# Kernel tuning notes

Measured on AMD Instinct MI355X. Metric: run time of the kernel, lower is better.

## Reference

```python
import jax, jax.numpy as jnp
import numpy as np

B, N, E, H = 4, 2048, 512, 8
D = E // H  # head dim = 64


def setup_inputs() -> dict:
    key = jax.random.key(0)
    ks = jax.random.split(key, 5)
    s = 1.0 / np.sqrt(E)
    return {
        "x": jax.random.normal(ks[0], (B, N, E), dtype=jnp.float32),
        "Wk": jax.random.normal(ks[1], (E, E), dtype=jnp.float32) * s,
        "bk": jax.random.normal(ks[2], (E,), dtype=jnp.float32) * s,
        "Wv": jax.random.normal(ks[3], (E, E), dtype=jnp.float32) * s,
        "bv": jax.random.normal(ks[4], (E,), dtype=jnp.float32) * s,
    }


def reference(x, Wk, bk, Wv, bv):
    b, n, e = x.shape
    # Linear projections (torch Linear: y = x @ W.T + b), split into heads.
    keys = (x @ Wk.T + bk).reshape(b, n, H, D).transpose(0, 2, 1, 3)    # b h n d
    values = (x @ Wv.T + bv).reshape(b, n, H, D).transpose(0, 2, 1, 3)  # b h n d
    # Q = K self-attention: scores [b, h, n, n]
    dotprod = jnp.einsum('bhnd,bhmd->bhnm', keys, keys)
    # softmax over last axis, then unusual POST-softmax scaling by sqrt(emb)
    att = jax.nn.softmax(dotprod, axis=-1) / jnp.sqrt(jnp.asarray(e, x.dtype))
    # dropout p=0 -> identity
    out = jnp.einsum('bhnm,bhmd->bhnd', att, values)
    return out.transpose(0, 2, 1, 3).reshape(b, n, e)
```

## Files before the change

kernel.cpp:

```cpp
#include <hip/hip_runtime.h>

typedef __bf16 bf16_t;
typedef bf16_t bf16x8 __attribute__((ext_vector_type(8)));
typedef float f32x4 __attribute__((ext_vector_type(4)));

#define NSEQ 2048
#define EMB 512
#define HEADS 8
#define HD 64
#define BATCH 4
#define LOG2E 1.4426950408889634f

#define MFMA16(a, b, c) __builtin_amdgcn_mfma_f32_16x16x32_bf16(a, b, c, 0, 0, 0)


__global__ __launch_bounds__(256, 2) void proj_kernel(
    const float* __restrict__ x,
    const float* __restrict__ Wk, const float* __restrict__ bk,
    const float* __restrict__ Wv, const float* __restrict__ bv,
    bf16_t* __restrict__ Kf, bf16_t* __restrict__ Vf)
{
  __shared__ union {
    struct {
      __align__(16) bf16_t A[2][128][40];
      __align__(16) bf16_t B[2][128][40];
    } s;
    __align__(16) bf16_t T[128][136];
  } u;

  const int t    = threadIdx.x;
  const int w    = t >> 6;
  const int lane = t & 63;
  const int quad = lane >> 4;
  const int l15  = lane & 15;
  const int wr   = w >> 1, wc = w & 1;
  const int m0   = blockIdx.x * 128;
  const int n0   = blockIdx.y * 128;
  const int zz   = (blockIdx.y >= 4);
  const float* __restrict__ W = zz ? Wv : Wk;
  const int nW = n0 - zz * 512;

  const int sr = t >> 3;
  const int sj = t & 7;
  const int sb = sj >> 2, sc = (sj & 3) * 8;

  float4 pa[4][2], pb[4][2];
  auto prefetch = [&](int k0) {
#pragma unroll
    for (int i = 0; i < 4; ++i) {
      const float* xa = x + (size_t)(m0 + sr + i * 32) * EMB + k0 + sj * 8;
      const float* wa = W + (size_t)(nW + sr + i * 32) * EMB + k0 + sj * 8;
      pa[i][0] = *(const float4*)xa; pa[i][1] = *(const float4*)(xa + 4);
      pb[i][0] = *(const float4*)wa; pb[i][1] = *(const float4*)(wa + 4);
    }
  };
  auto pack8 = [](float4 a, float4 b) -> bf16x8 {
    bf16x8 v;
    v[0] = (bf16_t)a.x; v[1] = (bf16_t)a.y; v[2] = (bf16_t)a.z; v[3] = (bf16_t)a.w;
    v[4] = (bf16_t)b.x; v[5] = (bf16_t)b.y; v[6] = (bf16_t)b.z; v[7] = (bf16_t)b.w;
    return v;
  };

  f32x4 acc[4][4] = {};
  prefetch(0);

  for (int it = 0; it < 8; ++it) {
    __syncthreads();
#pragma unroll
    for (int i = 0; i < 4; ++i) {
      *(bf16x8*)(&u.s.A[sb][sr + i * 32][sc]) = pack8(pa[i][0], pa[i][1]);
      *(bf16x8*)(&u.s.B[sb][sr + i * 32][sc]) = pack8(pb[i][0], pb[i][1]);
    }
    __syncthreads();
    if (it < 7) prefetch((it + 1) * 64);

    bf16x8 af[4][2], bf[4][2];
#pragma unroll
    for (int mt = 0; mt < 4; ++mt)
#pragma unroll
      for (int kk = 0; kk < 2; ++kk)
        af[mt][kk] = *(const bf16x8*)(&u.s.A[kk][wr * 64 + mt * 16 + l15][quad * 8]);
#pragma unroll
    for (int nt = 0; nt < 4; ++nt)
#pragma unroll
      for (int kk = 0; kk < 2; ++kk)
        bf[nt][kk] = *(const bf16x8*)(&u.s.B[kk][wc * 64 + nt * 16 + l15][quad * 8]);
#pragma unroll
    for (int kk = 0; kk < 2; ++kk)
#pragma unroll
      for (int mt = 0; mt < 4; ++mt)
#pragma unroll
        for (int nt = 0; nt < 4; ++nt)
          acc[mt][nt] = MFMA16(af[mt][kk], bf[nt][kk], acc[mt][nt]);
  }

  __syncthreads();

#pragma unroll
  for (int mt = 0; mt < 4; ++mt) {
#pragma unroll
    for (int nt = 0; nt < 4; ++nt) {
      const int F = wc * 64 + nt * 16 + l15;
      const int c = n0 + F;
      const float bb = zz ? bv[c - 512] : bk[c];
#pragma unroll
      for (int reg = 0; reg < 4; ++reg) {
        const int R = wr * 64 + mt * 16 + quad * 4 + reg;
        const float v = acc[mt][nt][reg] + bb;
        if (!zz) u.T[R][F] = (bf16_t)v;
        else     u.T[F][R] = (bf16_t)v;
      }
    }
  }
  __syncthreads();

  if (!zz) {
#pragma unroll
    for (int i = 0; i < 8; ++i) {
      const int fi  = i * 4 + w;
      const int hL  = fi >> 4, kk = (fi >> 3) & 1, ktl = fi & 7;
      const bf16x8 v = *(const bf16x8*)(&u.T[ktl * 16 + l15][hL * 64 + kk * 32 + quad * 8]);
      const int gr = m0 + ktl * 16 + l15;
      const int b = gr >> 11, n = gr & (NSEQ - 1);
      const int bh = b * HEADS + (n0 >> 6) + hL;
      bf16_t* dst = Kf + (((size_t)(bh * 128 + (n >> 4)) * 2 + kk)) * 512 + lane * 8;
      *(bf16x8*)dst = v;
    }
  } else {
#pragma unroll
    for (int i = 0; i < 8; ++i) {
      const int fi   = i * 4 + w;
      const int hL   = fi >> 4, dt = (fi >> 2) & 3, k32l = fi & 3;
      const bf16x8 v = *(const bf16x8*)(&u.T[hL * 64 + dt * 16 + l15][k32l * 32 + quad * 8]);
      const int gr = m0 + k32l * 32;
      const int b = gr >> 11, n = gr & (NSEQ - 1);
      const int bh = b * HEADS + ((n0 - 512) >> 6) + hL;
      bf16_t* dst = Vf + (((size_t)(bh * 64 + (n >> 5)) * 4 + dt)) * 512 + lane * 8;
      *(bf16x8*)dst = v;
    }
  }
}

__global__ __launch_bounds__(256, 2) void flash_kernel(
    const bf16_t* __restrict__ Kf, const bf16_t* __restrict__ Vf,
    float* __restrict__ out)
{
  __shared__ union {
    __align__(16) bf16_t Pl[4][64][40];
    struct {
      __align__(16) float Cb[2][4096];
      __align__(16) float Lb[2][64][16];
    } c;
  } u;

  const int t    = threadIdx.x;
  const int w    = t >> 6;
  const int lane = t & 63;
  const int quad = lane >> 4;
  const int l15  = lane & 15;
  const int rh   = w & 1;
  const int kh   = w >> 1;

  const int bh = blockIdx.x;
  const int b  = bh >> 3, h = bh & 7;
  const int rowbase = blockIdx.y * 128 + rh * 64;
  const int qtile   = rowbase >> 4;

  const bf16_t* __restrict__ Kb = Kf + (size_t)bh * 128 * 2 * 512;
  const bf16_t* __restrict__ Vb = Vf + (size_t)bh * 64 * 4 * 512;

  bf16x8 qf[4][2];
#pragma unroll
  for (int nt = 0; nt < 4; ++nt)
#pragma unroll
    for (int kk = 0; kk < 2; ++kk)
      qf[nt][kk] = *(const bf16x8*)(Kb + ((size_t)(qtile + nt) * 2 + kk) * 512 + lane * 8);

  float mlog[4];
#pragma unroll
  for (int nt = 0; nt < 4; ++nt) {
    float ss = 0.f;
#pragma unroll
    for (int kk = 0; kk < 2; ++kk)
#pragma unroll
      for (int j = 0; j < 8; ++j) {
        const float qv = (float)qf[nt][kk][j];
        ss = fmaf(qv, qv, ss);
      }
    ss += __shfl_xor(ss, 16, 64);
    ss += __shfl_xor(ss, 32, 64);
    mlog[nt] = ss * LOG2E;
  }

  bf16x8 ones;
#pragma unroll
  for (int j = 0; j < 8; ++j) ones[j] = (bf16_t)1.0f;

  f32x4 acco[4][4] = {};
  f32x4 accll[4]   = {};

  auto load_k = [&](int kt, bf16x8 (&dst)[2][2]) {
    const int kb = kt * 4 + kh * 2;
#pragma unroll
    for (int jt = 0; jt < 2; ++jt)
#pragma unroll
      for (int kk = 0; kk < 2; ++kk)
        dst[jt][kk] =
            *(const bf16x8*)(Kb + ((size_t)(kb + jt) * 2 + kk) * 512 + lane * 8);
  };

  auto body = [&](int kt, bf16x8 (&kcur)[2][2], bf16x8 (&knxt)[2][2]) {
    bf16x8 vf[4];
    const int v32 = kt * 2 + kh;
#pragma unroll
    for (int dt = 0; dt < 4; ++dt)
      vf[dt] = *(const bf16x8*)(Vb + ((size_t)v32 * 4 + dt) * 512 + lane * 8);

    f32x4 st[2][4] = {};
#pragma unroll
    for (int kk = 0; kk < 2; ++kk)
#pragma unroll
      for (int jt = 0; jt < 2; ++jt)
#pragma unroll
        for (int nt = 0; nt < 4; ++nt)
          st[jt][nt] = MFMA16(kcur[jt][kk], qf[nt][kk], st[jt][nt]);

    load_k(kt + 1 < NSEQ / 64 ? kt + 1 : kt, knxt);

#pragma unroll
    for (int jt = 0; jt < 2; ++jt)
#pragma unroll
      for (int nt = 0; nt < 4; ++nt) {
        union { bf16_t hx[4]; uint2 u2; } pw;
#pragma unroll
        for (int reg = 0; reg < 4; ++reg) {
          const float p =
              __builtin_amdgcn_exp2f(fmaf(st[jt][nt][reg], LOG2E, -mlog[nt]));
          pw.hx[reg] = (bf16_t)p;
        }
        *(uint2*)(&u.Pl[w][nt * 16 + l15][jt * 16 + quad * 4]) = pw.u2;
      }

    bf16x8 pf[4];
#pragma unroll
    for (int rt = 0; rt < 4; ++rt)
      pf[rt] = *(const bf16x8*)(&u.Pl[w][rt * 16 + l15][quad * 8]);
#pragma unroll
    for (int rt = 0; rt < 4; ++rt) {
      accll[rt] = MFMA16(pf[rt], ones, accll[rt]);
#pragma unroll
      for (int dt = 0; dt < 4; ++dt)
        acco[rt][dt] = MFMA16(pf[rt], vf[dt], acco[rt][dt]);
    }
  };

  bf16x8 kA[2][2], kB[2][2];
  load_k(0, kA);
  for (int kt = 0; kt < NSEQ / 64; kt += 2) {
    body(kt,     kA, kB);
    body(kt + 1, kB, kA);
  }

  __syncthreads();
  if (kh == 1) {
#pragma unroll
    for (int rt = 0; rt < 4; ++rt) {
#pragma unroll
      for (int dt = 0; dt < 4; ++dt)
        *(f32x4*)(&u.c.Cb[rh][((rt * 4 + dt) * 64 + lane) * 4]) = acco[rt][dt];
      *(f32x4*)(&u.c.Lb[rh][lane][rt * 4]) = accll[rt];
    }
  }
  __syncthreads();
  if (kh == 0) {
#pragma unroll
    for (int rt = 0; rt < 4; ++rt) {
#pragma unroll
      for (int dt = 0; dt < 4; ++dt)
        acco[rt][dt] += *(const f32x4*)(&u.c.Cb[rh][((rt * 4 + dt) * 64 + lane) * 4]);
      accll[rt] += *(const f32x4*)(&u.c.Lb[rh][lane][rt * 4]);
    }

    const float SCL = 0.044194173824159216f;
#pragma unroll
    for (int rt = 0; rt < 4; ++rt)
#pragma unroll
      for (int reg = 0; reg < 4; ++reg) {
        const float f = SCL / accll[rt][reg];
        const int n = rowbase + rt * 16 + quad * 4 + reg;
#pragma unroll
        for (int dt = 0; dt < 4; ++dt)
          out[((size_t)(b * NSEQ + n)) * EMB + h * HD + dt * 16 + l15] =
              acco[rt][dt][reg] * f;
      }
  }
}

extern "C" void kernel_launch(void* const* d_in, const int* in_sizes, int n_in,
                              void* d_out, int out_size, void* d_ws, size_t ws_size,
                              hipStream_t stream) {
  const float* x  = (const float*)d_in[0];
  const float* Wk = (const float*)d_in[1];
  const float* bk = (const float*)d_in[2];
  const float* Wv = (const float*)d_in[3];
  const float* bv = (const float*)d_in[4];
  float* out = (float*)d_out;

  bf16_t* Kf = (bf16_t*)d_ws;
  bf16_t* Vf = Kf + (size_t)BATCH * HEADS * NSEQ * HD;

  dim3 pg(8192 / 128, 1024 / 128);
  proj_kernel<<<pg, 256, 0, stream>>>(x, Wk, bk, Wv, bv, Kf, Vf);

  dim3 fg(BATCH * HEADS, NSEQ / 128);
  flash_kernel<<<fg, 256, 0, stream>>>(Kf, Vf, out);
}
```

Before: 129.9 us.

## Compute transposed PV with 16x16x16 MFMA directly from score registers, drop LDS P staging

```diff
diff --git a/kernel.cpp b/kernel.cpp
--- a/kernel.cpp
+++ b/kernel.cpp
@@ -3,6 +3,7 @@
 typedef __bf16 bf16_t;
 typedef bf16_t bf16x8 __attribute__((ext_vector_type(8)));
 typedef float f32x4 __attribute__((ext_vector_type(4)));
+typedef short s16x4 __attribute__((ext_vector_type(4)));
 
 #define NSEQ 2048
 #define EMB 512
@@ -12,6 +13,7 @@
 #define LOG2E 1.4426950408889634f
 
 #define MFMA16(a, b, c) __builtin_amdgcn_mfma_f32_16x16x32_bf16(a, b, c, 0, 0, 0)
+#define MFMA1K(a, b, c) __builtin_amdgcn_mfma_f32_16x16x16bf16_1k(a, b, c, 0, 0, 0)
 
 
 __global__ __launch_bounds__(256, 2) void proj_kernel(
@@ -131,12 +133,17 @@
     for (int i = 0; i < 8; ++i) {
       const int fi   = i * 4 + w;
       const int hL   = fi >> 4, dt = (fi >> 2) & 3, k32l = fi & 3;
-      const bf16x8 v = *(const bf16x8*)(&u.T[hL * 64 + dt * 16 + l15][k32l * 32 + quad * 8]);
+      const int F = hL * 64 + dt * 16 + l15;
+      union { bf16_t h[8]; bf16x8 v; } pk2;
+#pragma unroll
+      for (int jt = 0; jt < 2; ++jt)
+        *(uint2*)(&pk2.h[jt * 4]) =
+            *(const uint2*)(&u.T[F][k32l * 32 + jt * 16 + quad * 4]);
       const int gr = m0 + k32l * 32;
       const int b = gr >> 11, n = gr & (NSEQ - 1);
       const int bh = b * HEADS + ((n0 - 512) >> 6) + hL;
       bf16_t* dst = Vf + (((size_t)(bh * 64 + (n >> 5)) * 4 + dt)) * 512 + lane * 8;
-      *(bf16x8*)dst = v;
+      *(bf16x8*)dst = pk2.v;
     }
   }
 }
@@ -145,12 +152,9 @@
     const bf16_t* __restrict__ Kf, const bf16_t* __restrict__ Vf,
     float* __restrict__ out)
 {
-  __shared__ union {
-    __align__(16) bf16_t Pl[4][64][40];
-    struct {
-      __align__(16) float Cb[2][4096];
-      __align__(16) float Lb[2][64][16];
-    } c;
+  __shared__ struct {
+    __align__(16) float Cb[2][4096];
+    __align__(16) float Lb[2][64][4];
   } u;
 
   const int t    = threadIdx.x;
@@ -192,12 +196,8 @@
     mlog[nt] = ss * LOG2E;
   }
 
-  bf16x8 ones;
-#pragma unroll
-  for (int j = 0; j < 8; ++j) ones[j] = (bf16_t)1.0f;
-
-  f32x4 acco[4][4] = {};
-  f32x4 accll[4]   = {};
+  f32x4 accot[4][4] = {};
+  float lsum[4] = {0.f, 0.f, 0.f, 0.f};
 
   auto load_k = [&](int kt, bf16x8 (&dst)[2][2]) {
     const int kb = kt * 4 + kh * 2;
@@ -210,11 +210,11 @@
   };
 
   auto body = [&](int kt, bf16x8 (&kcur)[2][2], bf16x8 (&knxt)[2][2]) {
-    bf16x8 vf[4];
+    union { bf16x8 v8; s16x4 s4[2]; } vf[4];
     const int v32 = kt * 2 + kh;
 #pragma unroll
     for (int dt = 0; dt < 4; ++dt)
-      vf[dt] = *(const bf16x8*)(Vb + ((size_t)v32 * 4 + dt) * 512 + lane * 8);
+      vf[dt].v8 = *(const bf16x8*)(Vb + ((size_t)v32 * 4 + dt) * 512 + lane * 8);
 
     f32x4 st[2][4] = {};
 #pragma unroll
@@ -227,31 +227,29 @@
 
     load_k(kt + 1 < NSEQ / 64 ? kt + 1 : kt, knxt);
 
+    s16x4 pw[2][4];
 #pragma unroll
     for (int jt = 0; jt < 2; ++jt)
 #pragma unroll
       for (int nt = 0; nt < 4; ++nt) {
-        union { bf16_t hx[4]; uint2 u2; } pw;
+        union { bf16_t h[4]; s16x4 s; } pp;
 #pragma unroll
         for (int reg = 0; reg < 4; ++reg) {
           const float p =
               __builtin_amdgcn_exp2f(fmaf(st[jt][nt][reg], LOG2E, -mlog[nt]));
-          pw.hx[reg] = (bf16_t)p;
+          lsum[nt] += p;
+          pp.h[reg] = (bf16_t)p;
         }
-        *(uint2*)(&u.Pl[w][nt * 16 + l15][jt * 16 + quad * 4]) = pw.u2;
+        pw[jt][nt] = pp.s;
       }
 
-    bf16x8 pf[4];
-#pragma unroll
-    for (int rt = 0; rt < 4; ++rt)
-      pf[rt] = *(const bf16x8*)(&u.Pl[w][rt * 16 + l15][quad * 8]);
-#pragma unroll
-    for (int rt = 0; rt < 4; ++rt) {
-      accll[rt] = MFMA16(pf[rt], ones, accll[rt]);
+#pragma unroll
+    for (int jt = 0; jt < 2; ++jt)
 #pragma unroll
       for (int dt = 0; dt < 4; ++dt)
-        acco[rt][dt] = MFMA16(pf[rt], vf[dt], acco[rt][dt]);
-    }
+#pragma unroll
+        for (int nt = 0; nt < 4; ++nt)
+          accot[dt][nt] = MFMA1K(vf[dt].s4[jt], pw[jt][nt], accot[dt][nt]);
   };
 
   bf16x8 kA[2][2], kB[2][2];
@@ -264,35 +262,43 @@
   __syncthreads();
   if (kh == 1) {
 #pragma unroll
-    for (int rt = 0; rt < 4; ++rt) {
-#pragma unroll
-      for (int dt = 0; dt < 4; ++dt)
-        *(f32x4*)(&u.c.Cb[rh][((rt * 4 + dt) * 64 + lane) * 4]) = acco[rt][dt];
-      *(f32x4*)(&u.c.Lb[rh][lane][rt * 4]) = accll[rt];
-    }
+    for (int dt = 0; dt < 4; ++dt)
+#pragma unroll
+      for (int nt = 0; nt < 4; ++nt)
+        *(f32x4*)(&u.Cb[rh][((dt * 4 + nt) * 64 + lane) * 4]) = accot[dt][nt];
+#pragma unroll
+    for (int nt = 0; nt < 4; ++nt) u.Lb[rh][lane][nt] = lsum[nt];
   }
   __syncthreads();
   if (kh == 0) {
 #pragma unroll
-    for (int rt = 0; rt < 4; ++rt) {
-#pragma unroll
-      for (int dt = 0; dt < 4; ++dt)
-        acco[rt][dt] += *(const f32x4*)(&u.c.Cb[rh][((rt * 4 + dt) * 64 + lane) * 4]);
-      accll[rt] += *(const f32x4*)(&u.c.Lb[rh][lane][rt * 4]);
-    }
+    for (int dt = 0; dt < 4; ++dt)
+#pragma unroll
+      for (int nt = 0; nt < 4; ++nt)
+        accot[dt][nt] += *(const f32x4*)(&u.Cb[rh][((dt * 4 + nt) * 64 + lane) * 4]);
 
     const float SCL = 0.044194173824159216f;
-#pragma unroll
-    for (int rt = 0; rt < 4; ++rt)
-#pragma unroll
-      for (int reg = 0; reg < 4; ++reg) {
-        const float f = SCL / accll[rt][reg];
-        const int n = rowbase + rt * 16 + quad * 4 + reg;
-#pragma unroll
-        for (int dt = 0; dt < 4; ++dt)
-          out[((size_t)(b * NSEQ + n)) * EMB + h * HD + dt * 16 + l15] =
-              acco[rt][dt][reg] * f;
+    float f[4];
+#pragma unroll
+    for (int nt = 0; nt < 4; ++nt) {
+      float l = lsum[nt] + u.Lb[rh][lane][nt];
+      l += __shfl_xor(l, 16, 64);
+      l += __shfl_xor(l, 32, 64);
+      f[nt] = SCL / l;
+    }
+
+#pragma unroll
+    for (int nt = 0; nt < 4; ++nt) {
+      const int n = rowbase + nt * 16 + l15;
+      float* op = out + ((size_t)(b * NSEQ + n)) * EMB + h * HD;
+#pragma unroll
+      for (int dt = 0; dt < 4; ++dt) {
+        f32x4 v = accot[dt][nt];
+#pragma unroll
+        for (int reg = 0; reg < 4; ++reg) v[reg] *= f[nt];
+        *(f32x4*)(op + dt * 16 + quad * 4) = v;
       }
+    }
   }
 }
 
```

Measured after the change: 132.9 us. 2.2% more time.

## Split key sequence four ways per block with 64-row query tiles

Applied to the files above, without the earlier changes.

```diff
diff --git a/kernel.cpp b/kernel.cpp
--- a/kernel.cpp
+++ b/kernel.cpp
@@ -158,12 +158,11 @@
   const int lane = t & 63;
   const int quad = lane >> 4;
   const int l15  = lane & 15;
-  const int rh   = w & 1;
-  const int kh   = w >> 1;
+  const int kh   = w;
 
   const int bh = blockIdx.x;
   const int b  = bh >> 3, h = bh & 7;
-  const int rowbase = blockIdx.y * 128 + rh * 64;
+  const int rowbase = blockIdx.y * 64;
   const int qtile   = rowbase >> 4;
 
   const bf16_t* __restrict__ Kb = Kf + (size_t)bh * 128 * 2 * 512;
@@ -200,7 +199,7 @@
   f32x4 accll[4]   = {};
 
   auto load_k = [&](int kt, bf16x8 (&dst)[2][2]) {
-    const int kb = kt * 4 + kh * 2;
+    const int kb = kt * 8 + kh * 2;
 #pragma unroll
     for (int jt = 0; jt < 2; ++jt)
 #pragma unroll
@@ -211,7 +210,7 @@
 
   auto body = [&](int kt, bf16x8 (&kcur)[2][2], bf16x8 (&knxt)[2][2]) {
     bf16x8 vf[4];
-    const int v32 = kt * 2 + kh;
+    const int v32 = kt * 4 + kh;
 #pragma unroll
     for (int dt = 0; dt < 4; ++dt)
       vf[dt] = *(const bf16x8*)(Vb + ((size_t)v32 * 4 + dt) * 512 + lane * 8);
@@ -225,7 +224,7 @@
         for (int nt = 0; nt < 4; ++nt)
           st[jt][nt] = MFMA16(kcur[jt][kk], qf[nt][kk], st[jt][nt]);
 
-    load_k(kt + 1 < NSEQ / 64 ? kt + 1 : kt, knxt);
+    load_k(kt + 1 < 16 ? kt + 1 : kt, knxt);
 
 #pragma unroll
     for (int jt = 0; jt < 2; ++jt)
@@ -256,29 +255,50 @@
 
   bf16x8 kA[2][2], kB[2][2];
   load_k(0, kA);
-  for (int kt = 0; kt < NSEQ / 64; kt += 2) {
+  for (int kt = 0; kt < 16; kt += 2) {
     body(kt,     kA, kB);
     body(kt + 1, kB, kA);
   }
 
   __syncthreads();
-  if (kh == 1) {
-#pragma unroll
-    for (int rt = 0; rt < 4; ++rt) {
-#pragma unroll
-      for (int dt = 0; dt < 4; ++dt)
-        *(f32x4*)(&u.c.Cb[rh][((rt * 4 + dt) * 64 + lane) * 4]) = acco[rt][dt];
-      *(f32x4*)(&u.c.Lb[rh][lane][rt * 4]) = accll[rt];
-    }
-  }
-  __syncthreads();
-  if (kh == 0) {
-#pragma unroll
-    for (int rt = 0; rt < 4; ++rt) {
-#pragma unroll
-      for (int dt = 0; dt < 4; ++dt)
-        acco[rt][dt] += *(const f32x4*)(&u.c.Cb[rh][((rt * 4 + dt) * 64 + lane) * 4]);
-      accll[rt] += *(const f32x4*)(&u.c.Lb[rh][lane][rt * 4]);
+  if (w >= 2) {
+    const int s = w - 2;
+#pragma unroll
+    for (int rt = 0; rt < 4; ++rt) {
+#pragma unroll
+      for (int dt = 0; dt < 4; ++dt)
+        *(f32x4*)(&u.c.Cb[s][((rt * 4 + dt) * 64 + lane) * 4]) = acco[rt][dt];
+      *(f32x4*)(&u.c.Lb[s][lane][rt * 4]) = accll[rt];
+    }
+  }
+  __syncthreads();
+  if (w < 2) {
+#pragma unroll
+    for (int rt = 0; rt < 4; ++rt) {
+#pragma unroll
+      for (int dt = 0; dt < 4; ++dt)
+        acco[rt][dt] += *(const f32x4*)(&u.c.Cb[w][((rt * 4 + dt) * 64 + lane) * 4]);
+      accll[rt] += *(const f32x4*)(&u.c.Lb[w][lane][rt * 4]);
+    }
+  }
+  __syncthreads();
+  if (w == 1) {
+#pragma unroll
+    for (int rt = 0; rt < 4; ++rt) {
+#pragma unroll
+      for (int dt = 0; dt < 4; ++dt)
+        *(f32x4*)(&u.c.Cb[0][((rt * 4 + dt) * 64 + lane) * 4]) = acco[rt][dt];
+      *(f32x4*)(&u.c.Lb[0][lane][rt * 4]) = accll[rt];
+    }
+  }
+  __syncthreads();
+  if (w == 0) {
+#pragma unroll
+    for (int rt = 0; rt < 4; ++rt) {
+#pragma unroll
+      for (int dt = 0; dt < 4; ++dt)
+        acco[rt][dt] += *(const f32x4*)(&u.c.Cb[0][((rt * 4 + dt) * 64 + lane) * 4]);
+      accll[rt] += *(const f32x4*)(&u.c.Lb[0][lane][rt * 4]);
     }
 
     const float SCL = 0.044194173824159216f;
@@ -312,6 +332,6 @@
   dim3 pg(8192 / 128, 1024 / 128);
   proj_kernel<<<pg, 256, 0, stream>>>(x, Wk, bk, Wv, bv, Kf, Vf);
 
-  dim3 fg(BATCH * HEADS, NSEQ / 128);
+  dim3 fg(BATCH * HEADS, NSEQ / 64);
   flash_kernel<<<fg, 256, 0, stream>>>(Kf, Vf, out);
 }
```

After: 130.5 us. No clear change (+0.5%).
